# Optimization experiments

Hardware: AMD Instinct MI355X
Metric: run time of the kernel (lower is better)

Reference implementation:

```python
import jax, jax.numpy as jnp
import numpy as np

N, E, IN_DIM, H, D = 40000, 640000, 128, 8, 16


def setup_inputs() -> dict:
    key = jax.random.key(0)
    k_h, k_s, k_d, k_q, k_k, k_v = jax.random.split(key, 6)
    scale = float(np.sqrt(2.0 / (IN_DIM + H * D)))  # xavier-ish
    return {
        "h": jax.random.normal(k_h, (N, IN_DIM), dtype=jnp.float32),
        "src": jax.random.randint(k_s, (E,), 0, N, dtype=jnp.int32),
        "dst": jax.random.randint(k_d, (E,), 0, N, dtype=jnp.int32),
        "WQ": jax.random.normal(k_q, (IN_DIM, H * D), dtype=jnp.float32) * scale,
        "WK": jax.random.normal(k_k, (IN_DIM, H * D), dtype=jnp.float32) * scale,
        "WV": jax.random.normal(k_v, (IN_DIM, H * D), dtype=jnp.float32) * scale,
    }


def reference(h, src, dst, WQ, WK, WV):
    n = h.shape[0]
    Q = (h @ WQ).reshape(n, H, D)  # [N,H,D]
    K = (h @ WK).reshape(n, H, D)
    V = (h @ WV).reshape(n, H, D)
    inv_sqrt_d = 1.0 / jnp.sqrt(jnp.asarray(D, dtype=h.dtype))
    # per-edge elementwise score (DGL u_mul_v keeps the H x D vector)
    score = K[src] * Q[dst] * inv_sqrt_d  # [E,H,D]
    wV = jax.ops.segment_sum(V[src] * score, dst, num_segments=n)  # [N,H,D]
    z = jax.ops.segment_sum(score, dst, num_segments=n)            # [N,H,D]
    return wV / (z + 1e-6)
```

## Files before the change

kernel.cpp:

```cpp
#include <hip/hip_runtime.h>


#define FMA4(acc, s, b) do { \
    (acc).x = fmaf((s), (b).x, (acc).x); \
    (acc).y = fmaf((s), (b).y, (acc).y); \
    (acc).z = fmaf((s), (b).z, (acc).z); \
    (acc).w = fmaf((s), (b).w, (acc).w); } while (0)

__global__ __launch_bounds__(256) void gemm_qkv(
    const float* __restrict__ h,
    const float* __restrict__ WQ,
    const float* __restrict__ WK,
    const float* __restrict__ WV,
    float* __restrict__ Qf,
    float* __restrict__ KV,
    int N)
{
    __shared__ float4 Wl[32 * 32];
    __shared__ float4 Hl[128 * 8];
    const int t = threadIdx.x;
    const int which = blockIdx.y;
    const float* Wsel = (which == 0) ? WQ : ((which == 1) ? WK : WV);
    const float4* W4 = (const float4*)Wsel;
    const int r0 = blockIdx.x * 128;

    const int tc = t & 15;
    const int tr = t >> 4;

    float4 acc[8][2];
#pragma unroll
    for (int i = 0; i < 8; ++i) {
        acc[i][0] = make_float4(0.f, 0.f, 0.f, 0.f);
        acc[i][1] = make_float4(0.f, 0.f, 0.f, 0.f);
    }

    for (int kc = 0; kc < 4; ++kc) {
        __syncthreads();
#pragma unroll
        for (int i = 0; i < 4; ++i) {
            const int idx = t + i * 256;
            const int k = idx >> 5, c = idx & 31;
            Wl[idx] = W4[(size_t)(kc * 32 + k) * 32 + c];
        }
#pragma unroll
        for (int i = 0; i < 4; ++i) {
            const int idx = t + i * 256;
            const int row = idx >> 3, kk = idx & 7;
            float4 v = make_float4(0.f, 0.f, 0.f, 0.f);
            if (r0 + row < N)
                v = ((const float4*)h)[(size_t)(r0 + row) * 32 + kc * 8 + kk];
            Hl[row * 8 + (kk ^ ((row >> 3) & 7))] = v;
        }
        __syncthreads();

        for (int k4 = 0; k4 < 8; ++k4) {
            const float4 b0a = Wl[(k4 * 4 + 0) * 32 + tc];
            const float4 b0b = Wl[(k4 * 4 + 0) * 32 + tc + 16];
            const float4 b1a = Wl[(k4 * 4 + 1) * 32 + tc];
            const float4 b1b = Wl[(k4 * 4 + 1) * 32 + tc + 16];
            const float4 b2a = Wl[(k4 * 4 + 2) * 32 + tc];
            const float4 b2b = Wl[(k4 * 4 + 2) * 32 + tc + 16];
            const float4 b3a = Wl[(k4 * 4 + 3) * 32 + tc];
            const float4 b3b = Wl[(k4 * 4 + 3) * 32 + tc + 16];
#pragma unroll
            for (int r = 0; r < 8; ++r) {
                const int row = tr * 8 + r;
                const float4 a = Hl[row * 8 + (k4 ^ (tr & 7))];
                FMA4(acc[r][0], a.x, b0a); FMA4(acc[r][1], a.x, b0b);
                FMA4(acc[r][0], a.y, b1a); FMA4(acc[r][1], a.y, b1b);
                FMA4(acc[r][0], a.z, b2a); FMA4(acc[r][1], a.z, b2b);
                FMA4(acc[r][0], a.w, b3a); FMA4(acc[r][1], a.w, b3b);
            }
        }
    }

    if (which == 0) {
        float4* O = (float4*)Qf;
#pragma unroll
        for (int r = 0; r < 8; ++r) {
            const int row = r0 + tr * 8 + r;
            if (row < N) {
                O[(size_t)row * 32 + tc]      = acc[r][0];
                O[(size_t)row * 32 + tc + 16] = acc[r][1];
            }
        }
    } else {
        float2* O2 = (float2*)KV;
        const int voff = (which == 2) ? 1 : 0;
#pragma unroll
        for (int r = 0; r < 8; ++r) {
            const int row = r0 + tr * 8 + r;
            if (row < N) {
                const size_t base = (size_t)row * 128;
                O2[base + 4 * tc + 0 + voff]  = make_float2(acc[r][0].x, acc[r][0].y);
                O2[base + 4 * tc + 2 + voff]  = make_float2(acc[r][0].z, acc[r][0].w);
                O2[base + 4 * tc + 64 + voff] = make_float2(acc[r][1].x, acc[r][1].y);
                O2[base + 4 * tc + 66 + voff] = make_float2(acc[r][1].z, acc[r][1].w);
            }
        }
    }
}

__global__ __launch_bounds__(256) void count_deg(
    const int* __restrict__ dst, int* __restrict__ deg, int E)
{
    const int e = blockIdx.x * 256 + threadIdx.x;
    if (e < E) atomicAdd(&deg[dst[e]], 1);
}

__global__ __launch_bounds__(256) void chunk_reduce(
    const int* __restrict__ deg, int* __restrict__ csum, int N)
{
    const int t = threadIdx.x;
    const int i = blockIdx.x * 256 + t;
    int x = (i < N) ? deg[i] : 0;
#pragma unroll
    for (int off = 32; off; off >>= 1) x += __shfl_down(x, off, 64);
    __shared__ int ws[4];
    if ((t & 63) == 0) ws[t >> 6] = x;
    __syncthreads();
    if (t == 0) csum[blockIdx.x] = ws[0] + ws[1] + ws[2] + ws[3];
}

__global__ __launch_bounds__(256) void scan_chunks(
    const int* __restrict__ csum, int* __restrict__ coff, int nChunks)
{
    __shared__ int s[256];
    __shared__ int carry;
    const int t = threadIdx.x;
    if (t == 0) carry = 0;
    __syncthreads();
    for (int base = 0; base < nChunks; base += 256) {
        const int i = base + t;
        int x = (i < nChunks) ? csum[i] : 0;
        s[t] = x;
        __syncthreads();
        for (int off = 1; off < 256; off <<= 1) {
            int v = (t >= off) ? s[t - off] : 0;
            __syncthreads();
            s[t] += v;
            __syncthreads();
        }
        if (i < nChunks) coff[i] = carry + s[t] - x;
        __syncthreads();
        if (t == 0) carry += s[255];
        __syncthreads();
    }
}

__global__ __launch_bounds__(256) void chunk_scan(
    const int* __restrict__ deg, const int* __restrict__ coff,
    int* __restrict__ rowptr, int N)
{
    __shared__ int s[256];
    const int t = threadIdx.x;
    const int i = blockIdx.x * 256 + t;
    int x = (i < N) ? deg[i] : 0;
    s[t] = x;
    __syncthreads();
    for (int off = 1; off < 256; off <<= 1) {
        int v = (t >= off) ? s[t - off] : 0;
        __syncthreads();
        s[t] += v;
        __syncthreads();
    }
    if (i < N) rowptr[i + 1] = coff[blockIdx.x] + s[t];
    if (i == 0) rowptr[0] = 0;
}

__global__ __launch_bounds__(256) void scatter_eids(
    const int* __restrict__ dst, const int* __restrict__ rowptr,
    int* __restrict__ cur, int* __restrict__ eids, int E)
{
    const int e = blockIdx.x * 256 + threadIdx.x;
    if (e >= E) return;
    const int d = dst[e];
    const int pos = rowptr[d] + atomicAdd(&cur[d], 1);
    eids[pos] = e;
}

__global__ __launch_bounds__(256) void rank_emit(
    const int* __restrict__ rowptr, const int* __restrict__ eids,
    const int* __restrict__ src, int* __restrict__ srcs, int N)
{
    const int wave = threadIdx.x >> 6;
    const int lane = threadIdx.x & 63;
    const int d = blockIdx.x * 4 + wave;
    if (d >= N) return;
    const int lo = rowptr[d];
    const int deg = rowptr[d + 1] - lo;
    if (deg <= 64) {
        int p = 0x7fffffff;
        if (lane < deg) p = eids[lo + lane];
        int rank = 0;
        for (int j = 0; j < deg; ++j) {
            const int kj = __shfl(p, j, 64);
            rank += (kj < p) ? 1 : 0;
        }
        if (lane < deg) srcs[lo + rank] = src[p];
    } else if (lane == 0) {
        for (int i = 0; i < deg; ++i) {
            const int pi = eids[lo + i];
            int rank = 0;
            for (int j = 0; j < deg; ++j) rank += (eids[lo + j] < pi) ? 1 : 0;
            srcs[lo + rank] = src[pi];
        }
    }
}

__global__ __launch_bounds__(128) void attn_out(
    const int* __restrict__ srcs, const int* __restrict__ rowptr,
    const float* __restrict__ KV, const float* __restrict__ Qf,
    float* __restrict__ out, int N)
{
#pragma clang fp contract(off)
    const int wave = threadIdx.x >> 6;
    const int lane = threadIdx.x & 63;
    const int d = blockIdx.x * 2 + wave;
    if (d >= N) return;
    const float2 q = ((const float2*)Qf)[(size_t)d * 64 + lane];
    const int lo = rowptr[d], hi = rowptr[d + 1];
    const float4* KV4 = (const float4*)KV;
    float2 z = make_float2(0.f, 0.f), wv = z;

#define EDGE_UPD(kv) do { \
        float sc0 = ((kv).x * q.x) * 0.25f; z.x = z.x + sc0; wv.x = wv.x + (kv).z * sc0; \
        float sc1 = ((kv).y * q.y) * 0.25f; z.y = z.y + sc1; wv.y = wv.y + (kv).w * sc1; \
    } while (0)

    int i = lo;
    for (; i + 8 <= hi; i += 8) {
        int s[8];
#pragma unroll
        for (int u = 0; u < 8; ++u) s[u] = srcs[i + u];
        float4 kv[8];
#pragma unroll
        for (int u = 0; u < 8; ++u) kv[u] = KV4[(size_t)s[u] * 64 + lane];
#pragma unroll
        for (int u = 0; u < 8; ++u) EDGE_UPD(kv[u]);
    }
    for (; i + 4 <= hi; i += 4) {
        const int s0 = srcs[i + 0], s1 = srcs[i + 1];
        const int s2 = srcs[i + 2], s3 = srcs[i + 3];
        const float4 kv0 = KV4[(size_t)s0 * 64 + lane];
        const float4 kv1 = KV4[(size_t)s1 * 64 + lane];
        const float4 kv2 = KV4[(size_t)s2 * 64 + lane];
        const float4 kv3 = KV4[(size_t)s3 * 64 + lane];
        EDGE_UPD(kv0); EDGE_UPD(kv1); EDGE_UPD(kv2); EDGE_UPD(kv3);
    }
    for (; i < hi; ++i) {
        const float4 kv = KV4[(size_t)srcs[i] * 64 + lane];
        EDGE_UPD(kv);
    }
#undef EDGE_UPD

    float2 o;
    o.x = wv.x / (z.x + 1e-6f);
    o.y = wv.y / (z.y + 1e-6f);
    ((float2*)out)[(size_t)d * 64 + lane] = o;
}

extern "C" void kernel_launch(void* const* d_in, const int* in_sizes, int n_in,
                              void* d_out, int out_size, void* d_ws, size_t ws_size,
                              hipStream_t stream)
{
    const float* h  = (const float*)d_in[0];
    const int* src  = (const int*)d_in[1];
    const int* dst  = (const int*)d_in[2];
    const float* WQ = (const float*)d_in[3];
    const float* WK = (const float*)d_in[4];
    const float* WV = (const float*)d_in[5];
    const int N = in_sizes[0] / 128;
    const int E = in_sizes[1];
    const size_t NC = (size_t)N * 128;
    const int nChunks = (N + 255) / 256;

    float* KV = (float*)d_ws;
    float* Qf = KV + (size_t)N * 256;
    int* deg    = (int*)(Qf + NC);
    int* cur    = deg + N;
    int* rowptr = cur + N;
    int* csum   = rowptr + (N + 1);
    int* coff   = csum + nChunks;
    int* srcs   = coff + nChunks;
    int* eids   = srcs + E;
    float* outp = (float*)d_out;

    hipMemsetAsync(deg, 0, (size_t)2 * N * sizeof(int), stream);

    dim3 ggrid((N + 127) / 128, 3);
    gemm_qkv<<<ggrid, 256, 0, stream>>>(h, WQ, WK, WV, Qf, KV, N);

    const int eb = (E + 255) / 256;
    count_deg<<<eb, 256, 0, stream>>>(dst, deg, E);
    chunk_reduce<<<nChunks, 256, 0, stream>>>(deg, csum, N);
    scan_chunks<<<1, 256, 0, stream>>>(csum, coff, nChunks);
    chunk_scan<<<nChunks, 256, 0, stream>>>(deg, coff, rowptr, N);
    scatter_eids<<<eb, 256, 0, stream>>>(dst, rowptr, cur, eids, E);
    rank_emit<<<(N + 3) / 4, 256, 0, stream>>>(rowptr, eids, src, srcs, N);

    attn_out<<<(N + 1) / 2, 128, 0, stream>>>(srcs, rowptr, KV, Qf, outp, N);
}
```

Measured before the change: 304.5 us.

## Slice KV into head-group planes and degree-sort destinations for attention

The interleaved K/V buffer is stored as 8 slices, one per 16-float column group, so each destination's gather for a given slice touches a compact 128-byte row per source. The attention kernel now gives each 8-lane group one destination and one slice, and launches 8 blocks per group of 32 destinations. Destinations are ordered by a degree-bucketed permutation built from a histogram, a scan and a scatter, so lanes in a wave have similar loop trip counts. This adds three small kernels and removes the 8-wide unrolled loop, which lowers memory-level parallelism per lane. In exchange it aims for better cache locality per slice and less divergence within a wave.

Result: slower. 493.0 us (+61.9%).

```diff
diff --git a/kernel.cpp b/kernel.cpp
--- a/kernel.cpp
+++ b/kernel.cpp
@@ -13,7 +13,7 @@
     const float* __restrict__ WK,
     const float* __restrict__ WV,
     float* __restrict__ Qf,
-    float* __restrict__ KV,
+    float* __restrict__ KVs,
     int N)
 {
     __shared__ float4 Wl[32 * 32];
@@ -85,17 +85,20 @@
             }
         }
     } else {
-        float2* O2 = (float2*)KV;
+        float2* O2 = (float2*)KVs;
         const int voff = (which == 2) ? 1 : 0;
+        const int s0 = tc >> 2;
+        const int j0 = (2 * tc) & 7;
 #pragma unroll
         for (int r = 0; r < 8; ++r) {
             const int row = r0 + tr * 8 + r;
             if (row < N) {
-                const size_t base = (size_t)row * 128;
-                O2[base + 4 * tc + 0 + voff]  = make_float2(acc[r][0].x, acc[r][0].y);
-                O2[base + 4 * tc + 2 + voff]  = make_float2(acc[r][0].z, acc[r][0].w);
-                O2[base + 4 * tc + 64 + voff] = make_float2(acc[r][1].x, acc[r][1].y);
-                O2[base + 4 * tc + 66 + voff] = make_float2(acc[r][1].z, acc[r][1].w);
+                const size_t b0 = ((size_t)s0 * N + row) * 8;
+                const size_t b1 = ((size_t)(s0 + 4) * N + row) * 8;
+                O2[(b0 + j0)     * 2 + voff] = make_float2(acc[r][0].x, acc[r][0].y);
+                O2[(b0 + j0 + 1) * 2 + voff] = make_float2(acc[r][0].z, acc[r][0].w);
+                O2[(b1 + j0)     * 2 + voff] = make_float2(acc[r][1].x, acc[r][1].y);
+                O2[(b1 + j0 + 1) * 2 + voff] = make_float2(acc[r][1].z, acc[r][1].w);
             }
         }
     }
@@ -208,19 +211,62 @@
     }
 }
 
-__global__ __launch_bounds__(128) void attn_out(
+__global__ __launch_bounds__(256) void hist_deg(
+    const int* __restrict__ deg, int* __restrict__ hist, int N)
+{
+    const int n = blockIdx.x * 256 + threadIdx.x;
+    if (n < N) atomicAdd(&hist[min(deg[n], 127)], 1);
+}
+
+__global__ __launch_bounds__(128) void scan_hist(
+    const int* __restrict__ hist, int* __restrict__ binoff)
+{
+    __shared__ int s[128];
+    const int t = threadIdx.x;
+    const int x = hist[t];
+    s[t] = x;
+    __syncthreads();
+    for (int off = 1; off < 128; off <<= 1) {
+        int v = (t >= off) ? s[t - off] : 0;
+        __syncthreads();
+        s[t] += v;
+        __syncthreads();
+    }
+    binoff[t] = s[t] - x;
+}
+
+__global__ __launch_bounds__(256) void scatter_perm(
+    const int* __restrict__ deg, const int* __restrict__ binoff,
+    int* __restrict__ bincur, int* __restrict__ perm, int N)
+{
+    const int n = blockIdx.x * 256 + threadIdx.x;
+    if (n >= N) return;
+    const int b = min(deg[n], 127);
+    const int pos = binoff[b] + atomicAdd(&bincur[b], 1);
+    perm[pos] = n;
+}
+
+__global__ __launch_bounds__(256) void attn_out(
     const int* __restrict__ srcs, const int* __restrict__ rowptr,
-    const float* __restrict__ KV, const float* __restrict__ Qf,
+    const int* __restrict__ perm,
+    const float* __restrict__ KVs, const float* __restrict__ Qf,
     float* __restrict__ out, int N)
 {
 #pragma clang fp contract(off)
-    const int wave = threadIdx.x >> 6;
-    const int lane = threadIdx.x & 63;
-    const int d = blockIdx.x * 2 + wave;
-    if (d >= N) return;
-    const float2 q = ((const float2*)Qf)[(size_t)d * 64 + lane];
+    const int gid = blockIdx.x;
+    const int slice = gid & 7;
+    const int dblock = gid >> 3;
+    const int t = threadIdx.x;
+    const int wave = t >> 6;
+    const int lane = t & 63;
+    const int g = lane >> 3, j = lane & 7;
+    const int dstIdx = dblock * 32 + wave * 8 + g;
+    if (dstIdx >= N) return;
+    const int d = perm[dstIdx];
+    const float2 q = ((const float2*)Qf)[(size_t)d * 64 + slice * 8 + j];
     const int lo = rowptr[d], hi = rowptr[d + 1];
-    const float4* KV4 = (const float4*)KV;
+    const float4* KV4 = (const float4*)KVs;
+    const size_t sbase = (size_t)slice * N * 8 + j;
     float2 z = make_float2(0.f, 0.f), wv = z;
 
 #define EDGE_UPD(kv) do { \
@@ -229,27 +275,17 @@
     } while (0)
 
     int i = lo;
-    for (; i + 8 <= hi; i += 8) {
-        int s[8];
-#pragma unroll
-        for (int u = 0; u < 8; ++u) s[u] = srcs[i + u];
-        float4 kv[8];
-#pragma unroll
-        for (int u = 0; u < 8; ++u) kv[u] = KV4[(size_t)s[u] * 64 + lane];
-#pragma unroll
-        for (int u = 0; u < 8; ++u) EDGE_UPD(kv[u]);
-    }
     for (; i + 4 <= hi; i += 4) {
         const int s0 = srcs[i + 0], s1 = srcs[i + 1];
         const int s2 = srcs[i + 2], s3 = srcs[i + 3];
-        const float4 kv0 = KV4[(size_t)s0 * 64 + lane];
-        const float4 kv1 = KV4[(size_t)s1 * 64 + lane];
-        const float4 kv2 = KV4[(size_t)s2 * 64 + lane];
-        const float4 kv3 = KV4[(size_t)s3 * 64 + lane];
+        const float4 kv0 = KV4[sbase + (size_t)s0 * 8];
+        const float4 kv1 = KV4[sbase + (size_t)s1 * 8];
+        const float4 kv2 = KV4[sbase + (size_t)s2 * 8];
+        const float4 kv3 = KV4[sbase + (size_t)s3 * 8];
         EDGE_UPD(kv0); EDGE_UPD(kv1); EDGE_UPD(kv2); EDGE_UPD(kv3);
     }
     for (; i < hi; ++i) {
-        const float4 kv = KV4[(size_t)srcs[i] * 64 + lane];
+        const float4 kv = KV4[sbase + (size_t)srcs[i] * 8];
         EDGE_UPD(kv);
     }
 #undef EDGE_UPD
@@ -257,7 +293,7 @@
     float2 o;
     o.x = wv.x / (z.x + 1e-6f);
     o.y = wv.y / (z.y + 1e-6f);
-    ((float2*)out)[(size_t)d * 64 + lane] = o;
+    ((float2*)out)[(size_t)d * 64 + slice * 8 + j] = o;
 }
 
 extern "C" void kernel_launch(void* const* d_in, const int* in_sizes, int n_in,
@@ -275,29 +311,38 @@
     const size_t NC = (size_t)N * 128;
     const int nChunks = (N + 255) / 256;
 
-    float* KV = (float*)d_ws;
-    float* Qf = KV + (size_t)N * 256;
+    float* KVs = (float*)d_ws;
+    float* Qf  = KVs + (size_t)N * 256;
     int* deg    = (int*)(Qf + NC);
     int* cur    = deg + N;
-    int* rowptr = cur + N;
+    int* hist   = cur + N;
+    int* bincur = hist + 128;
+    int* binoff = bincur + 128;
+    int* perm   = binoff + 128;
+    int* rowptr = perm + N;
     int* csum   = rowptr + (N + 1);
     int* coff   = csum + nChunks;
     int* srcs   = coff + nChunks;
     int* eids   = srcs + E;
     float* outp = (float*)d_out;
 
-    hipMemsetAsync(deg, 0, (size_t)2 * N * sizeof(int), stream);
+    hipMemsetAsync(deg, 0, ((size_t)2 * N + 256) * sizeof(int), stream);
 
     dim3 ggrid((N + 127) / 128, 3);
-    gemm_qkv<<<ggrid, 256, 0, stream>>>(h, WQ, WK, WV, Qf, KV, N);
+    gemm_qkv<<<ggrid, 256, 0, stream>>>(h, WQ, WK, WV, Qf, KVs, N);
 
     const int eb = (E + 255) / 256;
+    const int nb = (N + 255) / 256;
     count_deg<<<eb, 256, 0, stream>>>(dst, deg, E);
     chunk_reduce<<<nChunks, 256, 0, stream>>>(deg, csum, N);
     scan_chunks<<<1, 256, 0, stream>>>(csum, coff, nChunks);
     chunk_scan<<<nChunks, 256, 0, stream>>>(deg, coff, rowptr, N);
     scatter_eids<<<eb, 256, 0, stream>>>(dst, rowptr, cur, eids, E);
     rank_emit<<<(N + 3) / 4, 256, 0, stream>>>(rowptr, eids, src, srcs, N);
-
-    attn_out<<<(N + 1) / 2, 128, 0, stream>>>(srcs, rowptr, KV, Qf, outp, N);
-}
+    hist_deg<<<nb, 256, 0, stream>>>(deg, hist, N);
+    scan_hist<<<1, 128, 0, stream>>>(hist, binoff);
+    scatter_perm<<<nb, 256, 0, stream>>>(deg, binoff, bincur, perm, N);
+
+    const int ndblocks = (N + 31) / 32;
+    attn_out<<<ndblocks * 8, 256, 0, stream>>>(srcs, rowptr, perm, KVs, Qf, outp, N);
+}
```
